# Performance work log

Measured on AMD Instinct MI355X. Metric: run time of the kernel, lower is better.

The kernel has to match this reference:

```python
import jax, jax.numpy as jnp
import numpy as np

SIGMA = 2.5
B, L, V, C = 8, 2048, 8192, 64
F = 2 * (C + 1)  # top_net in_features = 130


def rbf_interp(points_1, feats_1, points_2, sigma):
    """RBF interpolation of feats_1 at points_1 onto points_2 (atom2D torch_rbf, concat=True).
    points_1: [V,3], feats_1: [V,C], points_2: [L,3] -> [L, C+1]
    """
    # exact cdist via gram trick, [L, V]
    d2 = (jnp.sum(points_2 * points_2, -1)[:, None]
          - 2.0 * (points_2 @ points_1.T)
          + jnp.sum(points_1 * points_1, -1)[None, :])
    d = jnp.sqrt(jnp.maximum(d2, 0.0))
    w = jnp.exp(-d / sigma)                       # [L, V]
    dens = jnp.sum(w, axis=1, keepdims=True)      # [L, 1]
    w = w / dens
    # original computes weights under torch.no_grad()
    w = jax.lax.stop_gradient(w)
    dens = jax.lax.stop_gradient(dens)
    feats_2 = w @ feats_1                         # [L, C]
    return jnp.concatenate([feats_2, dens], axis=1)


def setup_inputs() -> dict:
    key = jax.random.key(0)
    ks = jax.random.split(key, 8)
    return {
        "locs_left": jax.random.normal(ks[0], (B, L, 3), jnp.float32),
        "locs_right": jax.random.normal(ks[1], (B, L, 3), jnp.float32),
        "verts_left": jax.random.normal(ks[2], (B, V, 3), jnp.float32),
        "verts_right": jax.random.normal(ks[3], (B, V, 3), jnp.float32),
        "feats_left": jax.random.normal(ks[4], (B, V, C), jnp.float32),
        "feats_right": jax.random.normal(ks[5], (B, V, C), jnp.float32),
        "w1": jax.random.normal(ks[6], (F, F), jnp.float32) * (1.0 / np.sqrt(F)),
        "b1": jnp.zeros((F,), jnp.float32),
        "w2": jax.random.normal(ks[7], (1, F), jnp.float32) * (1.0 / np.sqrt(F)),
        "b2": jnp.zeros((1,), jnp.float32),
    }


def reference(locs_left, locs_right, verts_left, verts_right,
              feats_left, feats_right, w1, b1, w2, b2):
    interp = jax.vmap(lambda p1, f1, p2: rbf_interp(p1, f1, p2, SIGMA))
    fl = interp(verts_left, feats_left, locs_left)     # [B, L, C+1]
    fr = interp(verts_right, feats_right, locs_right)  # [B, L, C+1]
    x = jnp.concatenate([fl, fr], axis=-1)             # [B, L, 2*(C+1)]
    h = jax.nn.relu(x @ w1.T + b1)                     # dropout inactive at eval
    out = h @ w2.T + b2                                # [B, L, 1]
    return out.reshape(-1)                             # [B*L]
```

## Files before the change

### kernel.cpp

```cpp
#include <hip/hip_runtime.h>
#include <hip/hip_bf16.h>
#include <stdint.h>

#define B_ 8
#define L_ 2048
#define V_ 8192
#define C_ 64
#define F_ 130

typedef float    f32x4  __attribute__((ext_vector_type(4)));
typedef float    f32x2  __attribute__((ext_vector_type(2)));
typedef short    s16x8  __attribute__((ext_vector_type(8)));
typedef __bf16   bf16x8 __attribute__((ext_vector_type(8)));
typedef uint32_t u32x4  __attribute__((ext_vector_type(4)));

#if __has_builtin(__builtin_amdgcn_exp2f)
#define EXP2(x) __builtin_amdgcn_exp2f(x)
#else
#define EXP2(x) exp2f(x)
#endif

__device__ __forceinline__ uint32_t pack2bf(float a, float b) {
  uint16_t ua = __builtin_bit_cast(uint16_t, (__bf16)a);
  uint16_t ub = __builtin_bit_cast(uint16_t, (__bf16)b);
  return (uint32_t)ua | ((uint32_t)ub << 16);
}

__device__ __forceinline__ float wave_sum(float v) {
  v += __shfl_xor(v, 1);  v += __shfl_xor(v, 2);  v += __shfl_xor(v, 4);
  v += __shfl_xor(v, 8);  v += __shfl_xor(v, 16); v += __shfl_xor(v, 32);
  return v;
}

__device__ __forceinline__ void gload_lds16(const void* g, void* l) {
  __builtin_amdgcn_global_load_lds(
      (const __attribute__((address_space(1))) void*)g,
      (__attribute__((address_space(3))) void*)l, 16, 0, 0);
}

__global__ __launch_bounds__(256) void pre_kernel(
    const float* __restrict__ verts_l, const float* __restrict__ verts_r,
    const float* __restrict__ feats_l, const float* __restrict__ feats_r,
    uint16_t* __restrict__ fT2, float* __restrict__ vS2)
{
  const int blk = blockIdx.x, tid = threadIdx.x;
  if (blk < 512) {
    const int p = blk >> 5, kt4 = blk & 31;
    const int side = p >> 3, bb = p & 7;
    const float* src = (side ? feats_r : feats_l) + (size_t)bb * (V_ * C_);
    const int sub = tid >> 6, t = tid & 63;
    const int ktile = kt4 * 4 + sub;
    const int ch = t >> 3;
    const int kq = (t & 7) ^ (ch & 7);
    const int k0 = ktile * 64 + kq * 8;
    float f[8];
    #pragma unroll
    for (int e = 0; e < 8; ++e) f[e] = src[(size_t)(k0 + e) * C_ + ch];
    u32x4 val = { pack2bf(f[0], f[1]), pack2bf(f[2], f[3]),
                  pack2bf(f[4], f[5]), pack2bf(f[6], f[7]) };
    char* dst = (char*)fT2 + ((size_t)p * 128 + ktile) * 8192 + t * 16;
    *(u32x4*)dst = val;
  } else {
    const int blk2 = blk - 512;
    const int p = blk2 >> 5, chunk = blk2 & 31;
    const int side = p >> 3, bb = p & 7;
    const float* src = (side ? verts_r : verts_l) + (size_t)bb * (V_ * 3);
    const int v = chunk * 256 + tid;
    const float x = src[v * 3 + 0], y = src[v * 3 + 1], z = src[v * 3 + 2];
    const float n2 = x * x + y * y + z * z;
    float* d = vS2 + (size_t)p * 32768 + (size_t)(v >> 6) * 256 + (v & 63);
    d[0] = x; d[64] = y; d[128] = z; d[192] = n2;
  }
}

__global__ __launch_bounds__(512, 2) void fused_kernel(
    const float* __restrict__ locs_l, const float* __restrict__ locs_r,
    const uint16_t* __restrict__ fT2, const float* __restrict__ vS2,
    const float* __restrict__ w1, const float* __restrict__ b1,
    const float* __restrict__ w2, const float* __restrict__ b2,
    float* __restrict__ outp)
{
  __shared__ __align__(16) char  flds[2][8192];
  __shared__ __align__(16) float vlds[2][4][64];
  __shared__ __align__(16) float xs[64][136];
  __shared__ float densp[64];

  const int bid  = blockIdx.x;
  const int bb   = bid & 7;
  const int tile = bid >> 3;
  const int tid  = threadIdx.x;
  const int wid  = tid >> 6, lane = tid & 63;
  const int g    = wid & 3, h = wid >> 2;
  const int ln15 = lane & 15, lg = lane >> 4;
  const int xorv = (ln15 & 7) << 4;
  constexpr float KEXP = -0.57707801635558535f;

  for (int s = 0; s < 2; ++s) {
    const int p = s * 8 + bb;
    const float* locs = (s ? locs_r : locs_l) + (size_t)bb * (L_ * 3);
    const int arow = tile * 64 + g * 16 + ln15;
    const float px = locs[arow * 3 + 0];
    const float py = locs[arow * 3 + 1];
    const float pz = locs[arow * 3 + 2];
    const float pn2 = px * px + py * py + pz * pz;

    const char* ftp = (const char*)fT2 + (size_t)p * (128 * 8192);
    const char* vtp = (const char*)vS2 + (size_t)p * (128 * 1024);

    f32x4 acc0 = {0.f,0.f,0.f,0.f}, acc1 = {0.f,0.f,0.f,0.f};
    f32x4 acc2 = {0.f,0.f,0.f,0.f}, acc3 = {0.f,0.f,0.f,0.f};
    float dens = 0.f;

    gload_lds16(ftp + wid * 1024 + lane * 16, &flds[0][wid * 1024]);
    if (wid == 0) gload_lds16(vtp + lane * 16, &vlds[0][0][0]);
    __syncthreads();

    for (int kt = 0; kt < 128; ++kt) {
      const int cur = kt & 1;
      if (kt < 127) {
        const int nxt = cur ^ 1;
        gload_lds16(ftp + (size_t)(kt + 1) * 8192 + wid * 1024 + lane * 16,
                    &flds[nxt][wid * 1024]);
        if (wid == 0)
          gload_lds16(vtp + (size_t)(kt + 1) * 1024 + lane * 16, &vlds[nxt][0][0]);
      }
      const int kof = h * 32 + lg * 8;
      const f32x4 vx0 = *(const f32x4*)&vlds[cur][0][kof];
      const f32x4 vx1 = *(const f32x4*)&vlds[cur][0][kof + 4];
      const f32x4 vy0 = *(const f32x4*)&vlds[cur][1][kof];
      const f32x4 vy1 = *(const f32x4*)&vlds[cur][1][kof + 4];
      const f32x4 vz0 = *(const f32x4*)&vlds[cur][2][kof];
      const f32x4 vz1 = *(const f32x4*)&vlds[cur][2][kof + 4];
      const f32x4 vn0 = *(const f32x4*)&vlds[cur][3][kof];
      const f32x4 vn1 = *(const f32x4*)&vlds[cur][3][kof + 4];
      bf16x8 av;
      #pragma unroll
      for (int e = 0; e < 8; ++e) {
        const float vx = (e < 4) ? vx0[e] : vx1[e - 4];
        const float vy = (e < 4) ? vy0[e] : vy1[e - 4];
        const float vz = (e < 4) ? vz0[e] : vz1[e - 4];
        const float vn = (e < 4) ? vn0[e] : vn1[e - 4];
        const float t2 = fmaf(px, vx, fmaf(py, vy, pz * vz));
        const float d2 = fmaf(-2.f, t2, pn2 + vn);
        const float d  = __builtin_amdgcn_sqrtf(fmaxf(d2, 0.f));
        const float w  = EXP2(d * KEXP);
        dens += w;
        av[e] = (__bf16)w;
      }
      const s16x8 afrag = __builtin_bit_cast(s16x8, av);
      const char* fl = flds[cur];
      const int ab = ln15 * 128 + (((h << 6) | (lg << 4)) ^ xorv);
      const s16x8 bf0 = *(const s16x8*)(fl + ab);
      const s16x8 bf1 = *(const s16x8*)(fl + ab + 2048);
      const s16x8 bf2 = *(const s16x8*)(fl + ab + 4096);
      const s16x8 bf3 = *(const s16x8*)(fl + ab + 6144);
      acc0 = __builtin_amdgcn_mfma_f32_16x16x32_bf16(afrag, bf0, acc0, 0, 0, 0);
      acc1 = __builtin_amdgcn_mfma_f32_16x16x32_bf16(afrag, bf1, acc1, 0, 0, 0);
      acc2 = __builtin_amdgcn_mfma_f32_16x16x32_bf16(afrag, bf2, acc2, 0, 0, 0);
      acc3 = __builtin_amdgcn_mfma_f32_16x16x32_bf16(afrag, bf3, acc3, 0, 0, 0);
      __syncthreads();
    }

    dens += __shfl_xor(dens, 16);
    dens += __shfl_xor(dens, 32);

    if (h == 0) {
      if (lane < 16) densp[g * 16 + lane] = dens;
      #pragma unroll
      for (int r = 0; r < 4; ++r) {
        const int row = g * 16 + lg * 4 + r;
        xs[row][s * 65 +      ln15] = acc0[r];
        xs[row][s * 65 + 16 + ln15] = acc1[r];
        xs[row][s * 65 + 32 + ln15] = acc2[r];
        xs[row][s * 65 + 48 + ln15] = acc3[r];
      }
    }
    __syncthreads();
    if (h == 1) {
      if (lane < 16) densp[g * 16 + lane] += dens;
      #pragma unroll
      for (int r = 0; r < 4; ++r) {
        const int row = g * 16 + lg * 4 + r;
        xs[row][s * 65 +      ln15] += acc0[r];
        xs[row][s * 65 + 16 + ln15] += acc1[r];
        xs[row][s * 65 + 32 + ln15] += acc2[r];
        xs[row][s * 65 + 48 + ln15] += acc3[r];
      }
    }
    __syncthreads();
    for (int idx = tid; idx < 64 * 64; idx += 512) {
      const int row = idx >> 6, c = idx & 63;
      xs[row][s * 65 + c] *= (1.0f / densp[row]);
    }
    if (tid < 64) xs[tid][s * 65 + 64] = densp[tid];
    __syncthreads();
  }

  const int r0 = wid * 8;
  float hh0[8], hh1[8];
  #pragma unroll
  for (int r = 0; r < 8; ++r) { hh0[r] = 0.f; hh1[r] = 0.f; }
  const float* wr0 = w1 + (size_t)lane * F_;
  const float* wr1 = w1 + (size_t)(lane + 64) * F_;

  #pragma unroll 4
  for (int i = 0; i < 128; i += 4) {
    const f32x2 a01 = *(const f32x2*)&wr0[i];
    const f32x2 a23 = *(const f32x2*)&wr0[i + 2];
    const f32x2 c01 = *(const f32x2*)&wr1[i];
    const f32x2 c23 = *(const f32x2*)&wr1[i + 2];
    #pragma unroll
    for (int r = 0; r < 8; ++r) {
      const f32x4 xv = *(const f32x4*)&xs[r0 + r][i];
      hh0[r] = fmaf(xv.x, a01.x, hh0[r]); hh0[r] = fmaf(xv.y, a01.y, hh0[r]);
      hh0[r] = fmaf(xv.z, a23.x, hh0[r]); hh0[r] = fmaf(xv.w, a23.y, hh0[r]);
      hh1[r] = fmaf(xv.x, c01.x, hh1[r]); hh1[r] = fmaf(xv.y, c01.y, hh1[r]);
      hh1[r] = fmaf(xv.z, c23.x, hh1[r]); hh1[r] = fmaf(xv.w, c23.y, hh1[r]);
    }
  }
  {
    const float a0 = wr0[128], a1 = wr0[129];
    const float c0 = wr1[128], c1 = wr1[129];
    #pragma unroll
    for (int r = 0; r < 8; ++r) {
      const float x0 = xs[r0 + r][128], x1 = xs[r0 + r][129];
      hh0[r] = fmaf(x0, a0, fmaf(x1, a1, hh0[r]));
      hh1[r] = fmaf(x0, c0, fmaf(x1, c1, hh1[r]));
    }
  }
  const float* wr2 = w1 + 128 * F_;
  const float* wr3 = w1 + 129 * F_;
  float hp2[8], hp3[8];
  #pragma unroll
  for (int r = 0; r < 8; ++r) {
    const float xa = xs[r0 + r][lane];
    const float xb = xs[r0 + r][lane + 64];
    float p2 = wr2[lane] * xa + wr2[lane + 64] * xb;
    float p3 = wr3[lane] * xa + wr3[lane + 64] * xb;
    if (lane < 2) {
      const float xc = xs[r0 + r][128 + lane];
      p2 += wr2[128 + lane] * xc;
      p3 += wr3[128 + lane] * xc;
    }
    hp2[r] = wave_sum(p2);
    hp3[r] = wave_sum(p3);
  }
  const float b1a = b1[lane], b1b = b1[lane + 64];
  const float w2a = w2[lane], w2b = w2[lane + 64];
  const float b1c = b1[128], b1d = b1[129];
  const float w2c = w2[128], w2d = w2[129];
  const float b2v = b2[0];
  #pragma unroll
  for (int r = 0; r < 8; ++r) {
    float o = w2a * fmaxf(hh0[r] + b1a, 0.f) + w2b * fmaxf(hh1[r] + b1b, 0.f);
    o = wave_sum(o);
    if (lane == 0) {
      o += w2c * fmaxf(hp2[r] + b1c, 0.f) + w2d * fmaxf(hp3[r] + b1d, 0.f);
      outp[(size_t)bb * L_ + tile * 64 + r0 + r] = o + b2v;
    }
  }
}

extern "C" void kernel_launch(void* const* d_in, const int* in_sizes, int n_in,
                              void* d_out, int out_size, void* d_ws, size_t ws_size,
                              hipStream_t stream) {
  const float* locs_l  = (const float*)d_in[0];
  const float* locs_r  = (const float*)d_in[1];
  const float* verts_l = (const float*)d_in[2];
  const float* verts_r = (const float*)d_in[3];
  const float* feats_l = (const float*)d_in[4];
  const float* feats_r = (const float*)d_in[5];
  const float* w1 = (const float*)d_in[6];
  const float* b1 = (const float*)d_in[7];
  const float* w2 = (const float*)d_in[8];
  const float* b2 = (const float*)d_in[9];

  char* ws = (char*)d_ws;
  uint16_t* fT2 = (uint16_t*)ws;
  float*    vS2 = (float*)(ws + 16777216);
  float*    out = (float*)d_out;

  pre_kernel<<<1024, 256, 0, stream>>>(verts_l, verts_r, feats_l, feats_r, fT2, vS2);
  fused_kernel<<<256, 512, 0, stream>>>(locs_l, locs_r, fT2, vS2,
                                        w1, b1, w2, b2, out);
}
```

Baseline: 251.9 us.

## Halve row tile, split K over four waves, stage pre-kernel transpose in LDS

The fused kernel now handles 32 query rows per block instead of 64 and launches 512 blocks to fill more CUs. Each block processes two K-tiles per iteration, with four wave groups splitting K and reducing in four phases. The distance/exp math uses packed float2 FMA/max to cut VALU instruction count. The pre-kernel now transposes features through a shared-memory tile with coalesced vector loads instead of strided scalar reads. The cost is more partial-sum reductions and barriers, and twice as many blocks re-reading the same feature data from L2.

Measured after the change: 225.0 us. 1.12x faster.

```diff
diff --git a/kernel.cpp b/kernel.cpp
--- a/kernel.cpp
+++ b/kernel.cpp
@@ -20,6 +20,21 @@
 #define EXP2(x) exp2f(x)
 #endif
 
+#if __has_builtin(__builtin_elementwise_fma)
+#define PK_FMA(a,b,c) __builtin_elementwise_fma((a),(b),(c))
+#else
+__device__ __forceinline__ f32x2 PK_FMA(f32x2 a, f32x2 b, f32x2 c) {
+  f32x2 r; r.x = fmaf(a.x,b.x,c.x); r.y = fmaf(a.y,b.y,c.y); return r;
+}
+#endif
+#if __has_builtin(__builtin_elementwise_max)
+#define PK_MAX(a,b) __builtin_elementwise_max((a),(b))
+#else
+__device__ __forceinline__ f32x2 PK_MAX(f32x2 a, f32x2 b) {
+  f32x2 r; r.x = fmaxf(a.x,b.x); r.y = fmaxf(a.y,b.y); return r;
+}
+#endif
+
 __device__ __forceinline__ uint32_t pack2bf(float a, float b) {
   uint16_t ua = __builtin_bit_cast(uint16_t, (__bf16)a);
   uint16_t ub = __builtin_bit_cast(uint16_t, (__bf16)b);
@@ -43,25 +58,44 @@
     const float* __restrict__ feats_l, const float* __restrict__ feats_r,
     uint16_t* __restrict__ fT2, float* __restrict__ vS2)
 {
+  __shared__ float fs[64][68];
   const int blk = blockIdx.x, tid = threadIdx.x;
-  if (blk < 512) {
-    const int p = blk >> 5, kt4 = blk & 31;
+  if (blk < 1024) {
+    const int p = blk >> 6, kt2 = blk & 63;
     const int side = p >> 3, bb = p & 7;
     const float* src = (side ? feats_r : feats_l) + (size_t)bb * (V_ * C_);
-    const int sub = tid >> 6, t = tid & 63;
-    const int ktile = kt4 * 4 + sub;
-    const int ch = t >> 3;
-    const int kq = (t & 7) ^ (ch & 7);
-    const int k0 = ktile * 64 + kq * 8;
-    float f[8];
+    const int r  = tid & 63;
+    const int eq = tid >> 6;
+    const int ch = r >> 3;
+    const int kq = (r & 7) ^ (ch & 7);
     #pragma unroll
-    for (int e = 0; e < 8; ++e) f[e] = src[(size_t)(k0 + e) * C_ + ch];
-    u32x4 val = { pack2bf(f[0], f[1]), pack2bf(f[2], f[3]),
-                  pack2bf(f[4], f[5]), pack2bf(f[6], f[7]) };
-    char* dst = (char*)fT2 + ((size_t)p * 128 + ktile) * 8192 + t * 16;
-    *(u32x4*)dst = val;
+    for (int sub = 0; sub < 2; ++sub) {
+      const int ktile = kt2 * 2 + sub;
+      const int v0 = ktile * 64;
+      {
+        const int sv = tid >> 2, c0 = (tid & 3) * 16;
+        const float* s = src + (size_t)(v0 + sv) * C_ + c0;
+        f32x4 a = *(const f32x4*)(s);
+        f32x4 b = *(const f32x4*)(s + 4);
+        f32x4 c = *(const f32x4*)(s + 8);
+        f32x4 d = *(const f32x4*)(s + 12);
+        *(f32x4*)&fs[sv][c0]      = a;
+        *(f32x4*)&fs[sv][c0 + 4]  = b;
+        *(f32x4*)&fs[sv][c0 + 8]  = c;
+        *(f32x4*)&fs[sv][c0 + 12] = d;
+      }
+      __syncthreads();
+      {
+        const int e = eq * 2;
+        const float f0 = fs[kq * 8 + e][ch];
+        const float f1 = fs[kq * 8 + e + 1][ch];
+        char* dst = (char*)fT2 + ((size_t)p * 128 + ktile) * 8192 + r * 16 + eq * 4;
+        *(uint32_t*)dst = pack2bf(f0, f1);
+      }
+      __syncthreads();
+    }
   } else {
-    const int blk2 = blk - 512;
+    const int blk2 = blk - 1024;
     const int p = blk2 >> 5, chunk = blk2 & 31;
     const int side = p >> 3, bb = p & 7;
     const float* src = (side ? verts_r : verts_l) + (size_t)bb * (V_ * 3);
@@ -73,87 +107,110 @@
   }
 }
 
-__global__ __launch_bounds__(512, 2) void fused_kernel(
+__global__ __launch_bounds__(512, 4) void fused_kernel(
     const float* __restrict__ locs_l, const float* __restrict__ locs_r,
     const uint16_t* __restrict__ fT2, const float* __restrict__ vS2,
     const float* __restrict__ w1, const float* __restrict__ b1,
     const float* __restrict__ w2, const float* __restrict__ b2,
     float* __restrict__ outp)
 {
-  __shared__ __align__(16) char  flds[2][8192];
-  __shared__ __align__(16) float vlds[2][4][64];
-  __shared__ __align__(16) float xs[64][136];
-  __shared__ float densp[64];
+  __shared__ __align__(16) char  flds[2][16384];
+  __shared__ __align__(16) float vlds[2][2][4][64];
+  __shared__ __align__(16) float xs[32][136];
+  __shared__ float densp[32];
 
   const int bid  = blockIdx.x;
   const int bb   = bid & 7;
   const int tile = bid >> 3;
   const int tid  = threadIdx.x;
   const int wid  = tid >> 6, lane = tid & 63;
-  const int g    = wid & 3, h = wid >> 2;
+  const int g    = wid & 1, h = wid >> 1;
   const int ln15 = lane & 15, lg = lane >> 4;
   const int xorv = (ln15 & 7) << 4;
   constexpr float KEXP = -0.57707801635558535f;
+  const f32x2 kexpv = {KEXP, KEXP};
+  const f32x2 m2v   = {-2.f, -2.f};
+  const f32x2 zerov = {0.f, 0.f};
+
+  const int sub  = h >> 1;
+  const int hh   = h & 1;
+  const int abfix = sub * 8192 + ln15 * 128 + ((((hh << 2) | lg) << 4) ^ xorv);
 
   for (int s = 0; s < 2; ++s) {
     const int p = s * 8 + bb;
     const float* locs = (s ? locs_r : locs_l) + (size_t)bb * (L_ * 3);
-    const int arow = tile * 64 + g * 16 + ln15;
+    const int arow = tile * 32 + g * 16 + ln15;
     const float px = locs[arow * 3 + 0];
     const float py = locs[arow * 3 + 1];
     const float pz = locs[arow * 3 + 2];
     const float pn2 = px * px + py * py + pz * pz;
+    const f32x2 pxv = {px, px}, pyv = {py, py}, pzv = {pz, pz};
+    const f32x2 pn2v = {pn2, pn2};
 
     const char* ftp = (const char*)fT2 + (size_t)p * (128 * 8192);
     const char* vtp = (const char*)vS2 + (size_t)p * (128 * 1024);
 
     f32x4 acc0 = {0.f,0.f,0.f,0.f}, acc1 = {0.f,0.f,0.f,0.f};
     f32x4 acc2 = {0.f,0.f,0.f,0.f}, acc3 = {0.f,0.f,0.f,0.f};
-    float dens = 0.f;
-
-    gload_lds16(ftp + wid * 1024 + lane * 16, &flds[0][wid * 1024]);
-    if (wid == 0) gload_lds16(vtp + lane * 16, &vlds[0][0][0]);
+    f32x2 densv = {0.f, 0.f};
+
+    gload_lds16(ftp + wid * 2048 + lane * 16,        &flds[0][wid * 2048]);
+    gload_lds16(ftp + wid * 2048 + 1024 + lane * 16, &flds[0][wid * 2048 + 1024]);
+    if (wid < 2) gload_lds16(vtp + wid * 1024 + lane * 16, &vlds[0][wid][0][0]);
     __syncthreads();
 
-    for (int kt = 0; kt < 128; ++kt) {
+    for (int kt = 0; kt < 64; ++kt) {
       const int cur = kt & 1;
-      if (kt < 127) {
+      if (kt < 63) {
         const int nxt = cur ^ 1;
-        gload_lds16(ftp + (size_t)(kt + 1) * 8192 + wid * 1024 + lane * 16,
-                    &flds[nxt][wid * 1024]);
-        if (wid == 0)
-          gload_lds16(vtp + (size_t)(kt + 1) * 1024 + lane * 16, &vlds[nxt][0][0]);
-      }
-      const int kof = h * 32 + lg * 8;
-      const f32x4 vx0 = *(const f32x4*)&vlds[cur][0][kof];
-      const f32x4 vx1 = *(const f32x4*)&vlds[cur][0][kof + 4];
-      const f32x4 vy0 = *(const f32x4*)&vlds[cur][1][kof];
-      const f32x4 vy1 = *(const f32x4*)&vlds[cur][1][kof + 4];
-      const f32x4 vz0 = *(const f32x4*)&vlds[cur][2][kof];
-      const f32x4 vz1 = *(const f32x4*)&vlds[cur][2][kof + 4];
-      const f32x4 vn0 = *(const f32x4*)&vlds[cur][3][kof];
-      const f32x4 vn1 = *(const f32x4*)&vlds[cur][3][kof + 4];
+        const char* gf = ftp + (size_t)(kt + 1) * 16384 + wid * 2048;
+        gload_lds16(gf + lane * 16,        &flds[nxt][wid * 2048]);
+        gload_lds16(gf + 1024 + lane * 16, &flds[nxt][wid * 2048 + 1024]);
+        if (wid < 2)
+          gload_lds16(vtp + (size_t)(kt + 1) * 2048 + wid * 1024 + lane * 16,
+                      &vlds[nxt][wid][0][0]);
+      }
+      const int kof = hh * 32 + lg * 8;
+      const f32x4 vx0 = *(const f32x4*)&vlds[cur][sub][0][kof];
+      const f32x4 vx1 = *(const f32x4*)&vlds[cur][sub][0][kof + 4];
+      const f32x4 vy0 = *(const f32x4*)&vlds[cur][sub][1][kof];
+      const f32x4 vy1 = *(const f32x4*)&vlds[cur][sub][1][kof + 4];
+      const f32x4 vz0 = *(const f32x4*)&vlds[cur][sub][2][kof];
+      const f32x4 vz1 = *(const f32x4*)&vlds[cur][sub][2][kof + 4];
+      const f32x4 vn0 = *(const f32x4*)&vlds[cur][sub][3][kof];
+      const f32x4 vn1 = *(const f32x4*)&vlds[cur][sub][3][kof + 4];
       bf16x8 av;
       #pragma unroll
-      for (int e = 0; e < 8; ++e) {
-        const float vx = (e < 4) ? vx0[e] : vx1[e - 4];
-        const float vy = (e < 4) ? vy0[e] : vy1[e - 4];
-        const float vz = (e < 4) ? vz0[e] : vz1[e - 4];
-        const float vn = (e < 4) ? vn0[e] : vn1[e - 4];
-        const float t2 = fmaf(px, vx, fmaf(py, vy, pz * vz));
-        const float d2 = fmaf(-2.f, t2, pn2 + vn);
-        const float d  = __builtin_amdgcn_sqrtf(fmaxf(d2, 0.f));
-        const float w  = EXP2(d * KEXP);
-        dens += w;
-        av[e] = (__bf16)w;
+      for (int pr = 0; pr < 4; ++pr) {
+        const f32x4 sx = (pr < 2) ? vx0 : vx1;
+        const f32x4 sy = (pr < 2) ? vy0 : vy1;
+        const f32x4 sz = (pr < 2) ? vz0 : vz1;
+        const f32x4 sn = (pr < 2) ? vn0 : vn1;
+        const int o = (pr & 1) * 2;
+        const f32x2 vx = {sx[o], sx[o + 1]};
+        const f32x2 vy = {sy[o], sy[o + 1]};
+        const f32x2 vz = {sz[o], sz[o + 1]};
+        const f32x2 vn = {sn[o], sn[o + 1]};
+        f32x2 t  = PK_FMA(pyv, vy, pzv * vz);
+        t        = PK_FMA(pxv, vx, t);
+        f32x2 d2 = PK_FMA(m2v, t, pn2v + vn);
+        d2       = PK_MAX(d2, zerov);
+        f32x2 dd;
+        dd.x = __builtin_amdgcn_sqrtf(d2.x);
+        dd.y = __builtin_amdgcn_sqrtf(d2.y);
+        dd = dd * kexpv;
+        const float w0 = EXP2(dd.x);
+        const float w1v = EXP2(dd.y);
+        densv += (f32x2){w0, w1v};
+        av[pr * 2]     = (__bf16)w0;
+        av[pr * 2 + 1] = (__bf16)w1v;
       }
       const s16x8 afrag = __builtin_bit_cast(s16x8, av);
       const char* fl = flds[cur];
-      const int ab = ln15 * 128 + (((h << 6) | (lg << 4)) ^ xorv);
-      const s16x8 bf0 = *(const s16x8*)(fl + ab);
-      const s16x8 bf1 = *(const s16x8*)(fl + ab + 2048);
-      const s16x8 bf2 = *(const s16x8*)(fl + ab + 4096);
-      const s16x8 bf3 = *(const s16x8*)(fl + ab + 6144);
+      const s16x8 bf0 = *(const s16x8*)(fl + abfix);
+      const s16x8 bf1 = *(const s16x8*)(fl + abfix + 2048);
+      const s16x8 bf2 = *(const s16x8*)(fl + abfix + 4096);
+      const s16x8 bf3 = *(const s16x8*)(fl + abfix + 6144);
       acc0 = __builtin_amdgcn_mfma_f32_16x16x32_bf16(afrag, bf0, acc0, 0, 0, 0);
       acc1 = __builtin_amdgcn_mfma_f32_16x16x32_bf16(afrag, bf1, acc1, 0, 0, 0);
       acc2 = __builtin_amdgcn_mfma_f32_16x16x32_bf16(afrag, bf2, acc2, 0, 0, 0);
@@ -161,45 +218,47 @@
       __syncthreads();
     }
 
+    float dens = densv.x + densv.y;
     dens += __shfl_xor(dens, 16);
     dens += __shfl_xor(dens, 32);
 
-    if (h == 0) {
-      if (lane < 16) densp[g * 16 + lane] = dens;
-      #pragma unroll
-      for (int r = 0; r < 4; ++r) {
-        const int row = g * 16 + lg * 4 + r;
-        xs[row][s * 65 +      ln15] = acc0[r];
-        xs[row][s * 65 + 16 + ln15] = acc1[r];
-        xs[row][s * 65 + 32 + ln15] = acc2[r];
-        xs[row][s * 65 + 48 + ln15] = acc3[r];
-      }
-    }
-    __syncthreads();
-    if (h == 1) {
-      if (lane < 16) densp[g * 16 + lane] += dens;
-      #pragma unroll
-      for (int r = 0; r < 4; ++r) {
-        const int row = g * 16 + lg * 4 + r;
-        xs[row][s * 65 +      ln15] += acc0[r];
-        xs[row][s * 65 + 16 + ln15] += acc1[r];
-        xs[row][s * 65 + 32 + ln15] += acc2[r];
-        xs[row][s * 65 + 48 + ln15] += acc3[r];
-      }
-    }
-    __syncthreads();
-    for (int idx = tid; idx < 64 * 64; idx += 512) {
+    #pragma unroll
+    for (int ph = 0; ph < 4; ++ph) {
+      if (h == ph) {
+        if (ph == 0) {
+          if (lane < 16) densp[g * 16 + lane] = dens;
+          #pragma unroll
+          for (int r = 0; r < 4; ++r) {
+            const int row = g * 16 + lg * 4 + r;
+            xs[row][s * 65 +      ln15] = acc0[r];
+            xs[row][s * 65 + 16 + ln15] = acc1[r];
+            xs[row][s * 65 + 32 + ln15] = acc2[r];
+            xs[row][s * 65 + 48 + ln15] = acc3[r];
+          }
+        } else {
+          if (lane < 16) densp[g * 16 + lane] += dens;
+          #pragma unroll
+          for (int r = 0; r < 4; ++r) {
+            const int row = g * 16 + lg * 4 + r;
+            xs[row][s * 65 +      ln15] += acc0[r];
+            xs[row][s * 65 + 16 + ln15] += acc1[r];
+            xs[row][s * 65 + 32 + ln15] += acc2[r];
+            xs[row][s * 65 + 48 + ln15] += acc3[r];
+          }
+        }
+      }
+      __syncthreads();
+    }
+    for (int idx = tid; idx < 32 * 64; idx += 512) {
       const int row = idx >> 6, c = idx & 63;
       xs[row][s * 65 + c] *= (1.0f / densp[row]);
     }
-    if (tid < 64) xs[tid][s * 65 + 64] = densp[tid];
+    if (tid < 32) xs[tid][s * 65 + 64] = densp[tid];
     __syncthreads();
   }
 
-  const int r0 = wid * 8;
-  float hh0[8], hh1[8];
-  #pragma unroll
-  for (int r = 0; r < 8; ++r) { hh0[r] = 0.f; hh1[r] = 0.f; }
+  const int r0 = wid * 4;
+  float hh0[4] = {0.f,0.f,0.f,0.f}, hh1[4] = {0.f,0.f,0.f,0.f};
   const float* wr0 = w1 + (size_t)lane * F_;
   const float* wr1 = w1 + (size_t)(lane + 64) * F_;
 
@@ -210,7 +269,7 @@
     const f32x2 c01 = *(const f32x2*)&wr1[i];
     const f32x2 c23 = *(const f32x2*)&wr1[i + 2];
     #pragma unroll
-    for (int r = 0; r < 8; ++r) {
+    for (int r = 0; r < 4; ++r) {
       const f32x4 xv = *(const f32x4*)&xs[r0 + r][i];
       hh0[r] = fmaf(xv.x, a01.x, hh0[r]); hh0[r] = fmaf(xv.y, a01.y, hh0[r]);
       hh0[r] = fmaf(xv.z, a23.x, hh0[r]); hh0[r] = fmaf(xv.w, a23.y, hh0[r]);
@@ -222,7 +281,7 @@
     const float a0 = wr0[128], a1 = wr0[129];
     const float c0 = wr1[128], c1 = wr1[129];
     #pragma unroll
-    for (int r = 0; r < 8; ++r) {
+    for (int r = 0; r < 4; ++r) {
       const float x0 = xs[r0 + r][128], x1 = xs[r0 + r][129];
       hh0[r] = fmaf(x0, a0, fmaf(x1, a1, hh0[r]));
       hh1[r] = fmaf(x0, c0, fmaf(x1, c1, hh1[r]));
@@ -230,9 +289,9 @@
   }
   const float* wr2 = w1 + 128 * F_;
   const float* wr3 = w1 + 129 * F_;
-  float hp2[8], hp3[8];
+  float hp2[4], hp3[4];
   #pragma unroll
-  for (int r = 0; r < 8; ++r) {
+  for (int r = 0; r < 4; ++r) {
     const float xa = xs[r0 + r][lane];
     const float xb = xs[r0 + r][lane + 64];
     float p2 = wr2[lane] * xa + wr2[lane + 64] * xb;
@@ -251,12 +310,12 @@
   const float w2c = w2[128], w2d = w2[129];
   const float b2v = b2[0];
   #pragma unroll
-  for (int r = 0; r < 8; ++r) {
+  for (int r = 0; r < 4; ++r) {
     float o = w2a * fmaxf(hh0[r] + b1a, 0.f) + w2b * fmaxf(hh1[r] + b1b, 0.f);
     o = wave_sum(o);
     if (lane == 0) {
       o += w2c * fmaxf(hp2[r] + b1c, 0.f) + w2d * fmaxf(hp3[r] + b1d, 0.f);
-      outp[(size_t)bb * L_ + tile * 64 + r0 + r] = o + b2v;
+      outp[(size_t)bb * L_ + tile * 32 + r0 + r] = o + b2v;
     }
   }
 }
@@ -280,7 +339,7 @@
   float*    vS2 = (float*)(ws + 16777216);
   float*    out = (float*)d_out;
 
-  pre_kernel<<<1024, 256, 0, stream>>>(verts_l, verts_r, feats_l, feats_r, fT2, vS2);
-  fused_kernel<<<256, 512, 0, stream>>>(locs_l, locs_r, fT2, vS2,
+  pre_kernel<<<1536, 256, 0, stream>>>(verts_l, verts_r, feats_l, feats_r, fT2, vS2);
+  fused_kernel<<<512, 512, 0, stream>>>(locs_l, locs_r, fT2, vS2,
                                         w1, b1, w2, b2, out);
 }
```
